# Kernel optimization log

Hardware: AMD Instinct MI355X
Metric: run time of the kernel (lower is better)

## Reference

```python
import jax, jax.numpy as jnp
import numpy as np

N, E, D = 50000, 400000, 64
L, NA, NS = 5, 4, 3            # layers, num aggregators, num scalers
ATOM_C, ATOM_V = 9, 64         # OGB-style atom feature columns / vocab
BOND_C, BOND_V = 3, 8
EPS = 1e-5
AVG_LOG = float(np.log(9.0))   # avg_d['log'] = ln(avg_degree + 1), avg_degree = 8


def setup_inputs() -> dict:
    key = jax.random.key(0)
    ks = jax.random.split(key, 8)
    x = jax.random.randint(ks[0], (N, ATOM_C), 0, ATOM_V)
    edge_index = jax.random.randint(ks[1], (2, E), 0, N)
    edge_attr = jax.random.randint(ks[2], (E, BOND_C), 0, BOND_V)
    init = lambda k, shape, fan: (jax.random.normal(k, shape, jnp.float32) / np.sqrt(fan))
    atom_emb = init(ks[3], (ATOM_C, ATOM_V, D), D)
    bond_emb = init(ks[4], (BOND_C, BOND_V, D), D)
    pre_W = init(ks[5], (L, 3 * D, D), 3 * D)                 # pretrans: Linear(3D -> D)
    pre_b = jnp.zeros((L, D), jnp.float32)
    post_W = init(ks[6], (L, (NA * NS + 1) * D, D), (NA * NS + 1) * D)  # posttrans: Linear(13D -> D)
    post_b = jnp.zeros((L, D), jnp.float32)
    return dict(x=x, edge_index=edge_index, edge_attr=edge_attr,
                atom_emb=atom_emb, bond_emb=bond_emb,
                pre_W=pre_W, pre_b=pre_b, post_W=post_W, post_b=post_b)


def reference(x, edge_index, edge_attr, atom_emb, bond_emb, pre_W, pre_b, post_W, post_b):
    src, dst = edge_index[0], edge_index[1]  # PyG: x_j = x[edge_index[0]], x_i = x[edge_index[1]]
    # Encoders: sum of per-column categorical embeddings (OGB Atom/BondEncoder)
    h0 = atom_emb[jnp.arange(ATOM_C)[None, :], x].sum(axis=1)        # [N, D]
    e = bond_emb[jnp.arange(BOND_C)[None, :], edge_attr].sum(axis=1)  # [E, D]
    # message input cat([x_i, x_j, edge_attr]) -- identical for every layer since
    # PNAGNN.forward never feeds layer output back in as x (faithful to source)
    z2 = jnp.concatenate([h0[dst], h0[src], e], axis=-1)              # [E, 3D]
    deg = jax.ops.segment_sum(jnp.ones((E,), jnp.float32), dst, num_segments=N)
    degc = jnp.maximum(deg, 1.0)[:, None]
    log_deg = jnp.log(jnp.maximum(deg, 1.0) + 1.0)[:, None]           # guard deg=0 for attenuation
    amp = log_deg / AVG_LOG
    att = AVG_LOG / log_deg
    has = (deg > 0)[:, None]
    h_in = h0
    for l in range(L):
        m = z2 @ pre_W[l] + pre_b[l]                                  # pretrans (1 layer, no act)
        s_sum = jax.ops.segment_sum(m, dst, num_segments=N)
        mean = s_sum / degc
        mx = jnp.where(has, jax.ops.segment_max(m, dst, num_segments=N), 0.0)
        mn = jnp.where(has, jax.ops.segment_min(m, dst, num_segments=N), 0.0)
        mean_sq = jax.ops.segment_sum(m * m, dst, num_segments=N) / degc
        var = jax.nn.relu(mean_sq - mean * mean)
        std = jnp.sqrt(var + EPS)
        agg = jnp.concatenate([mean, mx, mn, std], axis=-1)           # [N, 4D]
        scaled = jnp.concatenate([agg, agg * amp, agg * att], axis=-1)  # [N, 12D]
        hcat = jnp.concatenate([scaled, h0], axis=-1)                 # [N, 13D]
        out = hcat @ post_W[l] + post_b[l]                            # posttrans (1 layer, no act)
        h = out + h_in                                                # PNAGNN residual
        h_in = h
    return h
```

## Files before the change

kernel.cpp:

```cpp
#include <hip/hip_runtime.h>
#include <hip/hip_bf16.h>

#define NN 50000
#define NE 400000
#define AVG_LOG_F 2.1972245773362196f
#define EPSV 1e-5f

typedef __hip_bfloat16 bf16;
typedef __attribute__((ext_vector_type(8))) short short8v;
typedef __attribute__((ext_vector_type(4))) float f32x4;
typedef __attribute__((ext_vector_type(2))) _Float16 h2v;

__device__ __forceinline__ float b2f(bf16 v){ return __bfloat162float(v); }
__device__ __forceinline__ bf16  f2b(float v){ return __float2bfloat16(v); }
__device__ __forceinline__ short f2s(float v){
  bf16 b = __float2bfloat16(v);
  short s; __builtin_memcpy(&s, &b, 2); return s;
}
__device__ __forceinline__ float s2f(short v){
  bf16 b; __builtin_memcpy(&b, &v, 2); return __bfloat162float(b);
}

__global__ void k_h0(const int* __restrict__ x, const float* __restrict__ aemb,
                     bf16* __restrict__ h0b){
  int idx = blockIdx.x * 256 + threadIdx.x;
  if (idx >= NN * 64) return;
  int n = idx >> 6, d = idx & 63;
  float acc = 0.f;
  #pragma unroll
  for (int c = 0; c < 9; ++c){
    int a = x[n * 9 + c];
    acc += aemb[(c * 64 + a) * 64 + d];
  }
  h0b[idx] = f2b(acc);
}

__global__ void k_deg_code(const int* __restrict__ ei, const int* __restrict__ ea,
                           int* __restrict__ deg, int* __restrict__ code){
  int e = blockIdx.x * 256 + threadIdx.x;
  if (e >= NE) return;
  int dst = ei[NE + e];
  atomicAdd(&deg[dst], 1);
  code[e] = ea[e * 3] + 8 * ea[e * 3 + 1] + 64 * ea[e * 3 + 2];
}

__global__ void k_scan1(const int* __restrict__ deg, int* __restrict__ rowptr,
                        int* __restrict__ part){
  __shared__ int s[256];
  int t = threadIdx.x, i = blockIdx.x * 256 + t;
  int v = (i < NN) ? deg[i] : 0;
  s[t] = v; __syncthreads();
  for (int off = 1; off < 256; off <<= 1){
    int xv = (t >= off) ? s[t - off] : 0;
    __syncthreads();
    s[t] += xv;
    __syncthreads();
  }
  if (i < NN) rowptr[i] = s[t] - v;
  if (t == 255) part[blockIdx.x] = s[255];
}

__global__ void k_scan2(int* __restrict__ part, int nblk){
  __shared__ int s[256];
  int t = threadIdx.x;
  int v = (t < nblk) ? part[t] : 0;
  s[t] = v; __syncthreads();
  for (int off = 1; off < 256; off <<= 1){
    int xv = (t >= off) ? s[t - off] : 0;
    __syncthreads();
    s[t] += xv;
    __syncthreads();
  }
  if (t < nblk) part[t] = s[t] - v;
}

__global__ void k_scan3(int* __restrict__ rowptr, const int* __restrict__ part,
                        const int* __restrict__ deg, float* __restrict__ amp,
                        float* __restrict__ att){
  int i = blockIdx.x * 256 + threadIdx.x;
  if (i < NN){
    rowptr[i] += part[blockIdx.x];
    int d = deg[i];
    float ld = logf((float)max(d, 1) + 1.0f);
    amp[i] = ld / AVG_LOG_F;
    att[i] = AVG_LOG_F / ld;
  }
  if (i == 0) rowptr[NN] = NE;
}

__global__ void k_scatter(const int* __restrict__ ei, const int* __restrict__ code,
                          const int* __restrict__ rowptr, int* __restrict__ cursor,
                          int2* __restrict__ sedge){
  int e = blockIdx.x * 256 + threadIdx.x;
  if (e >= NE) return;
  int dst = ei[NE + e];
  int pos = rowptr[dst] + atomicAdd(&cursor[dst], 1);
  int2 v; v.x = ei[e]; v.y = code[e];
  sedge[pos] = v;
}

__global__ void k_ctab(const float* __restrict__ bemb, const float* __restrict__ preW,
                       _Float16* __restrict__ CTp){
  __shared__ float et[64];
  int cb = blockIdx.x, l = blockIdx.y, t = threadIdx.x;
  int a0 = cb & 7, a1 = (cb >> 3) & 7, a2 = (cb >> 6) & 7;
  et[t] = bemb[(0 * 8 + a0) * 64 + t] + bemb[(1 * 8 + a1) * 64 + t] + bemb[(2 * 8 + a2) * 64 + t];
  __syncthreads();
  float acc = 0.f;
  const float* W = preW + (l * 192 + 128) * 64;
  for (int k = 0; k < 64; ++k) acc += et[k] * W[k * 64 + t];
  CTp[((size_t)cb * 64 + t) * 8 + l] = (_Float16)acc;
}

__global__ void k_whsum(const float* __restrict__ postW, const float* __restrict__ postb,
                        float* __restrict__ whs, float* __restrict__ bs){
  int idx = blockIdx.x * 256 + threadIdx.x;
  if (idx < 4096){
    int k = idx >> 6, d = idx & 63;
    float a = 0.f;
    for (int l = 0; l < 5; ++l) a += postW[(size_t)(l * 832 + 768 + k) * 64 + d];
    whs[idx] = a;
  }
  if (idx < 64){
    float a = 0.f;
    for (int l = 0; l < 5; ++l) a += postb[l * 64 + idx];
    bs[idx] = a;
  }
}

__global__ void k_wtk(const float* __restrict__ postW, bf16* __restrict__ WtK){
  int idx = blockIdx.x * 256 + threadIdx.x;
  if (idx >= 3 * 64 * 1280) return;
  int g = idx / (64 * 1280);
  int rem = idx % (64 * 1280);
  int c = rem / 1280;
  int kk = rem % 1280;
  int l = kk >> 8, k = kk & 255;
  WtK[idx] = f2b(postW[((size_t)l * 832 + g * 256 + k) * 64 + c]);
}

__global__ void k_wtpre896(const float* __restrict__ preW, const float* __restrict__ preb,
                           const float* __restrict__ whs, const float* __restrict__ bs,
                           bf16* __restrict__ Wtp, float* __restrict__ bias896){
  int idx = blockIdx.x * 256 + threadIdx.x;
  if (idx < 896 * 64){
    int gc = idx >> 6, k = idx & 63;
    float v;
    if (gc < 320){
      int l = gc >> 6, c = gc & 63;
      v = preW[(size_t)(l * 192 + k) * 64 + c];
    } else if (gc < 832){
      int q = gc - 320, d = q >> 3, l = q & 7;
      v = (l < 5) ? preW[(size_t)(l * 192 + 64 + k) * 64 + d] : 0.f;
    } else {
      int c = gc - 832;
      v = whs[k * 64 + c] + ((k == c) ? 1.f : 0.f);
    }
    Wtp[idx] = f2b(v);
  }
  if (idx < 896){
    float b;
    if (idx < 320)      b = preb[(idx >> 6) * 64 + (idx & 63)];
    else if (idx < 832) b = 0.f;
    else                b = bs[idx - 832];
    bias896[idx] = b;
  }
}

__global__ __launch_bounds__(256) void k_ab_mfma(const bf16* __restrict__ h0b,
                                                 const bf16* __restrict__ Wtp,
                                                 const float* __restrict__ bias896,
                                                 _Float16* __restrict__ ABU,
                                                 float* __restrict__ out){
  __shared__ bf16 As[128][72];
  __shared__ bf16 Bs[128][72];
  const int t = threadIdx.x;
  const int n0 = blockIdx.x * 128;
  const int gc0 = blockIdx.y * 128;
  const int lane = t & 63, wid = t >> 6;
  const int rw = wid * 32;
  const short* H  = (const short*)h0b;
  const short* Wp = (const short*)Wtp;

  #pragma unroll
  for (int i = 0; i < 4; ++i){
    int idx = t + i * 256;
    int r = idx >> 3, ko = (idx & 7) * 8;
    int n = n0 + r;
    short8v v = short8v{0,0,0,0,0,0,0,0};
    if (n < NN) v = *(const short8v*)(H + (size_t)n * 64 + ko);
    *(short8v*)&As[r][ko] = v;
  }
  #pragma unroll
  for (int i = 0; i < 4; ++i){
    int idx = t + i * 256;
    int cc = idx >> 3, ko = (idx & 7) * 8;
    *(short8v*)&Bs[cc][ko] = *(const short8v*)(Wp + (size_t)(gc0 + cc) * 64 + ko);
  }
  __syncthreads();

  f32x4 acc[2][8] = {};
  #pragma unroll
  for (int kk = 0; kk < 2; ++kk){
    short8v af0 = *(const short8v*)&As[rw + (lane & 15)][kk * 32 + (lane >> 4) * 8];
    short8v af1 = *(const short8v*)&As[rw + 16 + (lane & 15)][kk * 32 + (lane >> 4) * 8];
    #pragma unroll
    for (int j = 0; j < 8; ++j){
      short8v bfj = *(const short8v*)&Bs[j * 16 + (lane & 15)][kk * 32 + (lane >> 4) * 8];
      acc[0][j] = __builtin_amdgcn_mfma_f32_16x16x32_bf16(af0, bfj, acc[0][j], 0, 0, 0);
      acc[1][j] = __builtin_amdgcn_mfma_f32_16x16x32_bf16(af1, bfj, acc[1][j], 0, 0, 0);
    }
  }

  #pragma unroll
  for (int i = 0; i < 2; ++i){
    #pragma unroll
    for (int r = 0; r < 4; ++r){
      int n = n0 + rw + i * 16 + (lane >> 4) * 4 + r;
      if (n >= NN) continue;
      #pragma unroll
      for (int j = 0; j < 8; ++j){
        int gc = gc0 + j * 16 + (lane & 15);
        float v = acc[i][j][r] + bias896[gc];
        if (gc < 832) ABU[(size_t)n * 832 + gc] = (_Float16)v;
        else          out[(size_t)n * 64 + (gc - 832)] = v;
      }
    }
  }
}

__global__ __launch_bounds__(256) void k_gather(const _Float16* __restrict__ ABU,
                                                const _Float16* __restrict__ CTp,
                                                const int* __restrict__ rowptr,
                                                const int2* __restrict__ sedge,
                                                bf16* __restrict__ AGG){
  const int t = threadIdx.x, lane = t & 63, wid = t >> 6;
  const int n = blockIdx.x * 4 + wid;
  const short* ABUs = (const short*)ABU;
  const short* CTps = (const short*)CTp;
  short* AGs = (short*)AGG;

  int r0 = rowptr[n], r1 = rowptr[n + 1];
  float s[5]  = {0.f, 0.f, 0.f, 0.f, 0.f};
  float sq[5] = {0.f, 0.f, 0.f, 0.f, 0.f};
  const _Float16 FLO = (_Float16)(-65504.f);
  const _Float16 FHI = (_Float16)( 65504.f);
  h2v mx01 = h2v{FLO, FLO}, mx23 = h2v{FLO, FLO}, mx45 = h2v{FLO, FLO};
  h2v mn01 = h2v{FHI, FHI}, mn23 = h2v{FHI, FHI}, mn45 = h2v{FHI, FHI};

  union P8 { short8v s; h2v h[4]; };

  for (int j = r0; j < r1; j += 4){
    int rem = r1 - j;
    int2 e0 = sedge[j];
    int2 e1 = (rem > 1) ? sedge[j + 1] : e0;
    int2 e2 = (rem > 2) ? sedge[j + 2] : e0;
    int2 e3 = (rem > 3) ? sedge[j + 3] : e0;
    P8 a0, c0, a1, c1, a2, c2, a3, c3;
    a0.s = *(const short8v*)(ABUs + (size_t)e0.x * 832 + 320 + lane * 8);
    c0.s = *(const short8v*)(CTps + (size_t)e0.y * 512 + lane * 8);
    a1.s = *(const short8v*)(ABUs + (size_t)e1.x * 832 + 320 + lane * 8);
    c1.s = *(const short8v*)(CTps + (size_t)e1.y * 512 + lane * 8);
    a2.s = *(const short8v*)(ABUs + (size_t)e2.x * 832 + 320 + lane * 8);
    c2.s = *(const short8v*)(CTps + (size_t)e2.y * 512 + lane * 8);
    a3.s = *(const short8v*)(ABUs + (size_t)e3.x * 832 + 320 + lane * 8);
    c3.s = *(const short8v*)(CTps + (size_t)e3.y * 512 + lane * 8);

    #define EDGE_ACC(A, C) {                                        \
      h2v t01 = A.h[0] + C.h[0];                                    \
      h2v t23 = A.h[1] + C.h[1];                                    \
      h2v t45 = A.h[2] + C.h[2];                                    \
      mx01 = __builtin_elementwise_max(mx01, t01);                  \
      mx23 = __builtin_elementwise_max(mx23, t23);                  \
      mx45 = __builtin_elementwise_max(mx45, t45);                  \
      mn01 = __builtin_elementwise_min(mn01, t01);                  \
      mn23 = __builtin_elementwise_min(mn23, t23);                  \
      mn45 = __builtin_elementwise_min(mn45, t45);                  \
      float f0 = (float)t01[0], f1 = (float)t01[1];                 \
      float f2 = (float)t23[0], f3 = (float)t23[1];                 \
      float f4 = (float)t45[0];                                     \
      s[0] += f0; sq[0] = fmaf(f0, f0, sq[0]);                      \
      s[1] += f1; sq[1] = fmaf(f1, f1, sq[1]);                      \
      s[2] += f2; sq[2] = fmaf(f2, f2, sq[2]);                      \
      s[3] += f3; sq[3] = fmaf(f3, f3, sq[3]);                      \
      s[4] += f4; sq[4] = fmaf(f4, f4, sq[4]);                      \
    }
    EDGE_ACC(a0, c0);
    if (rem > 1) EDGE_ACC(a1, c1);
    if (rem > 2) EDGE_ACC(a2, c2);
    if (rem > 3) EDGE_ACC(a3, c3);
    #undef EDGE_ACC
  }

  float mx[5] = {(float)mx01[0], (float)mx01[1], (float)mx23[0], (float)mx23[1], (float)mx45[0]};
  float mn[5] = {(float)mn01[0], (float)mn01[1], (float)mn23[0], (float)mn23[1], (float)mn45[0]};

  int d = r1 - r0;
  float degc = (float)((d > 0) ? d : 1);
  size_t base = (size_t)n * 1280;
  #pragma unroll
  for (int l = 0; l < 5; ++l){
    float K = (float)ABU[(size_t)n * 832 + l * 64 + lane];
    float mean = ((float)d * K + s[l]) / degc;
    float MX = (d > 0) ? (K + mx[l]) : 0.f;
    float MN = (d > 0) ? (K + mn[l]) : 0.f;
    float mu = s[l] / degc;
    float var = fmaxf(sq[l] / degc - mu * mu, 0.f);
    float sd = sqrtf(var + EPSV);
    AGs[base + l * 256 + lane]       = f2s(mean);
    AGs[base + l * 256 + 64 + lane]  = f2s(MX);
    AGs[base + l * 256 + 128 + lane] = f2s(MN);
    AGs[base + l * 256 + 192 + lane] = f2s(sd);
  }
}

__global__ __launch_bounds__(512) void k_post5(const bf16* __restrict__ AGG,
                                               const bf16* __restrict__ WtK,
                                               const float* __restrict__ amp,
                                               const float* __restrict__ att,
                                               float* __restrict__ out){
  __shared__ short As[2][128][140];
  const int t = threadIdx.x, lane = t & 63, wid = t >> 6;
  const int n0 = blockIdx.x * 128;
  const int w4 = wid & 3, rh = wid >> 2;
  const short* AGs = (const short*)AGG;
  const short* Ws  = (const short*)WtK;
  const short8v zv = short8v{0,0,0,0,0,0,0,0};

  #pragma unroll
  for (int i = 0; i < 4; ++i){
    int id = t + i * 512;
    int r = id >> 4, ko = (id & 15) * 8;
    int n = n0 + r;
    short8v v = zv;
    if (n < NN) v = *(const short8v*)(AGs + (size_t)n * 1280 + ko);
    *(short8v*)&As[0][r][ko] = v;
  }
  __syncthreads();

  f32x4 acc[4][3] = {};
  for (int kt = 0; kt < 10; ++kt){
    const int cur = kt & 1;
    short8v pref[4];
    if (kt < 9){
      #pragma unroll
      for (int i = 0; i < 4; ++i){
        int id = t + i * 512;
        int r = id >> 4, ko = (id & 15) * 8;
        int n = n0 + r;
        pref[i] = zv;
        if (n < NN) pref[i] = *(const short8v*)(AGs + (size_t)n * 1280 + (kt + 1) * 128 + ko);
      }
    }
    #pragma unroll
    for (int kk = 0; kk < 4; ++kk){
      short8v bfg[3];
      #pragma unroll
      for (int g = 0; g < 3; ++g)
        bfg[g] = *(const short8v*)(Ws + (size_t)(g * 64 + w4 * 16 + (lane & 15)) * 1280 +
                                   kt * 128 + kk * 32 + (lane >> 4) * 8);
      #pragma unroll
      for (int rf = 0; rf < 4; ++rf){
        short8v af = *(const short8v*)&As[cur][rh * 64 + rf * 16 + (lane & 15)]
                                         [kk * 32 + (lane >> 4) * 8];
        #pragma unroll
        for (int g = 0; g < 3; ++g)
          acc[rf][g] = __builtin_amdgcn_mfma_f32_16x16x32_bf16(af, bfg[g], acc[rf][g], 0, 0, 0);
      }
    }
    if (kt < 9){
      #pragma unroll
      for (int i = 0; i < 4; ++i){
        int id = t + i * 512;
        int r = id >> 4, ko = (id & 15) * 8;
        *(short8v*)&As[cur ^ 1][r][ko] = pref[i];
      }
    }
    __syncthreads();
  }

  #pragma unroll
  for (int rf = 0; rf < 4; ++rf){
    #pragma unroll
    for (int r = 0; r < 4; ++r){
      int n = n0 + rh * 64 + rf * 16 + (lane >> 4) * 4 + r;
      if (n >= NN) continue;
      float am = amp[n], at = att[n];
      int c = w4 * 16 + (lane & 15);
      out[(size_t)n * 64 + c] += acc[rf][0][r] + am * acc[rf][1][r] + at * acc[rf][2][r];
    }
  }
}

extern "C" void kernel_launch(void* const* d_in, const int* in_sizes, int n_in,
                              void* d_out, int out_size, void* d_ws, size_t ws_size,
                              hipStream_t stream){
  const int*   x     = (const int*)d_in[0];
  const int*   ei    = (const int*)d_in[1];
  const int*   ea    = (const int*)d_in[2];
  const float* aemb  = (const float*)d_in[3];
  const float* bemb  = (const float*)d_in[4];
  const float* preW  = (const float*)d_in[5];
  const float* preb  = (const float*)d_in[6];
  const float* postW = (const float*)d_in[7];
  const float* postb = (const float*)d_in[8];
  float* out = (float*)d_out;

  char* p = (char*)d_ws;
  auto alloc = [&](size_t bytes) -> char* {
    char* r = p;
    p += (bytes + 255) & ~(size_t)255;
    return r;
  };
  bf16*      h0b     = (bf16*)     alloc((size_t)NN * 64 * 2);
  _Float16*  ABU     = (_Float16*) alloc((size_t)NN * 832 * 2);
  bf16*      AGG     = (bf16*)     alloc((size_t)NN * 1280 * 2);
  int*       deg     = (int*)      alloc((size_t)NN * 4);
  int*       rowptr  = (int*)      alloc((size_t)(NN + 1) * 4);
  int*       cursor  = (int*)      alloc((size_t)NN * 4);
  float*     amp     = (float*)    alloc((size_t)NN * 4);
  float*     att     = (float*)    alloc((size_t)NN * 4);
  int*       code    = (int*)      alloc((size_t)NE * 4);
  int2*      sedge   = (int2*)     alloc((size_t)NE * 8);
  _Float16*  CTp     = (_Float16*) alloc((size_t)512 * 64 * 8 * 2 + 64);
  float*     whs     = (float*)    alloc((size_t)64 * 64 * 4);
  float*     bs      = (float*)    alloc((size_t)64 * 4);
  int*       part    = (int*)      alloc((size_t)256 * 4);
  bf16*      WtK     = (bf16*)     alloc((size_t)3 * 64 * 1280 * 2);
  bf16*      Wtp     = (bf16*)     alloc((size_t)896 * 64 * 2);
  float*     bias896 = (float*)    alloc((size_t)896 * 4);
  if ((size_t)(p - (char*)d_ws) > ws_size) return;

  hipMemsetAsync(deg, 0, (size_t)NN * 4, stream);
  hipMemsetAsync(cursor, 0, (size_t)NN * 4, stream);

  k_h0<<<dim3((NN * 64 + 255) / 256), 256, 0, stream>>>(x, aemb, h0b);
  k_deg_code<<<dim3((NE + 255) / 256), 256, 0, stream>>>(ei, ea, deg, code);
  int nblk = (NN + 255) / 256;
  k_scan1<<<dim3(nblk), 256, 0, stream>>>(deg, rowptr, part);
  k_scan2<<<dim3(1), 256, 0, stream>>>(part, nblk);
  k_scan3<<<dim3(nblk), 256, 0, stream>>>(rowptr, part, deg, amp, att);
  k_scatter<<<dim3((NE + 255) / 256), 256, 0, stream>>>(ei, code, rowptr, cursor, sedge);
  k_ctab<<<dim3(512, 5), 64, 0, stream>>>(bemb, preW, CTp);
  k_whsum<<<dim3(16), 256, 0, stream>>>(postW, postb, whs, bs);
  k_wtk<<<dim3((3 * 64 * 1280 + 255) / 256), 256, 0, stream>>>(postW, WtK);
  k_wtpre896<<<dim3((896 * 64 + 255) / 256), 256, 0, stream>>>(preW, preb, whs, bs,
                                                               Wtp, bias896);
  k_ab_mfma<<<dim3((NN + 127) / 128, 7), 256, 0, stream>>>(h0b, Wtp, bias896, ABU, out);
  k_gather<<<dim3(NN / 4), 256, 0, stream>>>(ABU, CTp, rowptr, sedge, AGG);
  k_post5<<<dim3((NN + 127) / 128), 512, 0, stream>>>(AGG, WtK, amp, att, out);
}
```

Measured before the change: 290.5 us.

## Split post-transform GEMM over K across blocks with atomic adds; precompute gather byte offsets

```diff
diff --git a/kernel.cpp b/kernel.cpp
--- a/kernel.cpp
+++ b/kernel.cpp
@@ -95,7 +95,7 @@
   if (e >= NE) return;
   int dst = ei[NE + e];
   int pos = rowptr[dst] + atomicAdd(&cursor[dst], 1);
-  int2 v; v.x = ei[e]; v.y = code[e];
+  int2 v; v.x = ei[e] * 1664 + 640; v.y = code[e] * 1024;
   sedge[pos] = v;
 }
 
@@ -236,8 +236,8 @@
                                                 bf16* __restrict__ AGG){
   const int t = threadIdx.x, lane = t & 63, wid = t >> 6;
   const int n = blockIdx.x * 4 + wid;
-  const short* ABUs = (const short*)ABU;
-  const short* CTps = (const short*)CTp;
+  const char* ABUb = (const char*)ABU;
+  const char* CTpb = (const char*)CTp;
   short* AGs = (short*)AGG;
 
   int r0 = rowptr[n], r1 = rowptr[n + 1];
@@ -249,6 +249,7 @@
   h2v mn01 = h2v{FHI, FHI}, mn23 = h2v{FHI, FHI}, mn45 = h2v{FHI, FHI};
 
   union P8 { short8v s; h2v h[4]; };
+  const int lb = lane * 16;
 
   for (int j = r0; j < r1; j += 4){
     int rem = r1 - j;
@@ -257,14 +258,14 @@
     int2 e2 = (rem > 2) ? sedge[j + 2] : e0;
     int2 e3 = (rem > 3) ? sedge[j + 3] : e0;
     P8 a0, c0, a1, c1, a2, c2, a3, c3;
-    a0.s = *(const short8v*)(ABUs + (size_t)e0.x * 832 + 320 + lane * 8);
-    c0.s = *(const short8v*)(CTps + (size_t)e0.y * 512 + lane * 8);
-    a1.s = *(const short8v*)(ABUs + (size_t)e1.x * 832 + 320 + lane * 8);
-    c1.s = *(const short8v*)(CTps + (size_t)e1.y * 512 + lane * 8);
-    a2.s = *(const short8v*)(ABUs + (size_t)e2.x * 832 + 320 + lane * 8);
-    c2.s = *(const short8v*)(CTps + (size_t)e2.y * 512 + lane * 8);
-    a3.s = *(const short8v*)(ABUs + (size_t)e3.x * 832 + 320 + lane * 8);
-    c3.s = *(const short8v*)(CTps + (size_t)e3.y * 512 + lane * 8);
+    a0.s = *(const short8v*)(ABUb + e0.x + lb);
+    c0.s = *(const short8v*)(CTpb + e0.y + lb);
+    a1.s = *(const short8v*)(ABUb + e1.x + lb);
+    c1.s = *(const short8v*)(CTpb + e1.y + lb);
+    a2.s = *(const short8v*)(ABUb + e2.x + lb);
+    c2.s = *(const short8v*)(CTpb + e2.y + lb);
+    a3.s = *(const short8v*)(ABUb + e3.x + lb);
+    c3.s = *(const short8v*)(CTpb + e3.y + lb);
 
     #define EDGE_ACC(A, C) {                                        \
       h2v t01 = A.h[0] + C.h[0];                                    \
@@ -319,39 +320,30 @@
                                                const float* __restrict__ amp,
                                                const float* __restrict__ att,
                                                float* __restrict__ out){
-  __shared__ short As[2][128][140];
+  __shared__ short As[128][140];
   const int t = threadIdx.x, lane = t & 63, wid = t >> 6;
   const int n0 = blockIdx.x * 128;
+  const int ks = blockIdx.y;
   const int w4 = wid & 3, rh = wid >> 2;
   const short* AGs = (const short*)AGG;
   const short* Ws  = (const short*)WtK;
   const short8v zv = short8v{0,0,0,0,0,0,0,0};
 
-  #pragma unroll
-  for (int i = 0; i < 4; ++i){
-    int id = t + i * 512;
-    int r = id >> 4, ko = (id & 15) * 8;
-    int n = n0 + r;
-    short8v v = zv;
-    if (n < NN) v = *(const short8v*)(AGs + (size_t)n * 1280 + ko);
-    *(short8v*)&As[0][r][ko] = v;
-  }
-  __syncthreads();
-
   f32x4 acc[4][3] = {};
-  for (int kt = 0; kt < 10; ++kt){
-    const int cur = kt & 1;
-    short8v pref[4];
-    if (kt < 9){
-      #pragma unroll
-      for (int i = 0; i < 4; ++i){
-        int id = t + i * 512;
-        int r = id >> 4, ko = (id & 15) * 8;
-        int n = n0 + r;
-        pref[i] = zv;
-        if (n < NN) pref[i] = *(const short8v*)(AGs + (size_t)n * 1280 + (kt + 1) * 128 + ko);
-      }
-    }
+  #pragma unroll
+  for (int kt2 = 0; kt2 < 2; ++kt2){
+    const int kt = ks * 2 + kt2;
+    if (kt2) __syncthreads();
+    #pragma unroll
+    for (int i = 0; i < 4; ++i){
+      int id = t + i * 512;
+      int r = id >> 4, ko = (id & 15) * 8;
+      int n = n0 + r;
+      short8v v = zv;
+      if (n < NN) v = *(const short8v*)(AGs + (size_t)n * 1280 + kt * 128 + ko);
+      *(short8v*)&As[r][ko] = v;
+    }
+    __syncthreads();
     #pragma unroll
     for (int kk = 0; kk < 4; ++kk){
       short8v bfg[3];
@@ -361,22 +353,13 @@
                                    kt * 128 + kk * 32 + (lane >> 4) * 8);
       #pragma unroll
       for (int rf = 0; rf < 4; ++rf){
-        short8v af = *(const short8v*)&As[cur][rh * 64 + rf * 16 + (lane & 15)]
+        short8v af = *(const short8v*)&As[rh * 64 + rf * 16 + (lane & 15)]
                                          [kk * 32 + (lane >> 4) * 8];
         #pragma unroll
         for (int g = 0; g < 3; ++g)
           acc[rf][g] = __builtin_amdgcn_mfma_f32_16x16x32_bf16(af, bfg[g], acc[rf][g], 0, 0, 0);
       }
     }
-    if (kt < 9){
-      #pragma unroll
-      for (int i = 0; i < 4; ++i){
-        int id = t + i * 512;
-        int r = id >> 4, ko = (id & 15) * 8;
-        *(short8v*)&As[cur ^ 1][r][ko] = pref[i];
-      }
-    }
-    __syncthreads();
   }
 
   #pragma unroll
@@ -387,7 +370,8 @@
       if (n >= NN) continue;
       float am = amp[n], at = att[n];
       int c = w4 * 16 + (lane & 15);
-      out[(size_t)n * 64 + c] += acc[rf][0][r] + am * acc[rf][1][r] + at * acc[rf][2][r];
+      float v = acc[rf][0][r] + am * acc[rf][1][r] + at * acc[rf][2][r];
+      atomicAdd(&out[(size_t)n * 64 + c], v);
     }
   }
 }
@@ -448,5 +432,5 @@
                                                                Wtp, bias896);
   k_ab_mfma<<<dim3((NN + 127) / 128, 7), 256, 0, stream>>>(h0b, Wtp, bias896, ABU, out);
   k_gather<<<dim3(NN / 4), 256, 0, stream>>>(ABU, CTp, rowptr, sedge, AGG);
-  k_post5<<<dim3((NN + 127) / 128), 512, 0, stream>>>(AGG, WtK, amp, att, out);
-}
+  k_post5<<<dim3((NN + 127) / 128, 5), 512, 0, stream>>>(AGG, WtK, amp, att, out);
+}
```

Result: slower. 309.2 us (+6.4%).
